# Performance work log

Hardware: AMD Instinct MI355X
Metric: run time of the kernel (lower is better)

## Reference

```python
import jax, jax.numpy as jnp
import numpy as np


def setup_inputs() -> dict:
    key = jax.random.key(0)
    ks = jax.random.split(key, 5)
    B, C, H, W = 4, 256, 48, 48
    x = jax.random.normal(ks[0], (B, C, H, W), dtype=jnp.float32)
    w_qkv = jax.random.normal(ks[1], (3 * C, C), dtype=jnp.float32) * (C ** -0.5)
    b_qkv = jax.random.normal(ks[2], (3 * C,), dtype=jnp.float32) * 0.02
    w_proj = jax.random.normal(ks[3], (C, C), dtype=jnp.float32) * (C ** -0.5)
    b_proj = jax.random.normal(ks[4], (C,), dtype=jnp.float32) * 0.02
    return {"x": x, "w_qkv": w_qkv, "b_qkv": b_qkv, "w_proj": w_proj, "b_proj": b_proj, "num_heads": 4}


def reference(x, w_qkv, b_qkv, w_proj, b_proj, num_heads):
    B, C, H, W = x.shape
    N = H * W
    hd = C // num_heads
    # NOTE: original uses full-dim scale, not head_dim
    scale = C ** -0.5
    # 1x1 conv == channel matmul
    qkv = jnp.einsum('bchw,oc->bohw', x, w_qkv) + b_qkv[None, :, None, None]
    qkv = qkv.reshape(B, 3, num_heads, hd, N)
    q = qkv[:, 0].transpose(0, 1, 3, 2)  # [B, h, N, d]
    k = qkv[:, 1]                         # [B, h, d, N]
    v = qkv[:, 2].transpose(0, 1, 3, 2)  # [B, h, N, d]
    attn = jax.nn.softmax((q @ k) * scale, axis=-1)  # [B, h, N, N]
    out = attn @ v                        # [B, h, N, d]
    out = out.transpose(0, 1, 3, 2).reshape(B, C, H, W)
    return jnp.einsum('bchw,oc->bohw', out, w_proj) + b_proj[None, :, None, None]
```

## Files before the change

### kernel.cpp

```cpp
#include <hip/hip_runtime.h>
#include <hip/hip_bf16.h>
#include <stdint.h>

typedef unsigned short u16;
typedef unsigned int u32;
typedef __attribute__((ext_vector_type(8))) short bf16x8;
typedef __attribute__((ext_vector_type(4))) float f32x4;
typedef __attribute__((ext_vector_type(4))) unsigned short u16x4;

#define MFMA16 __builtin_amdgcn_mfma_f32_16x16x32_bf16

static constexpr int Bb = 4;
static constexpr int Cc = 256;
static constexpr int NHh = 4;
static constexpr int HDd = 64;
static constexpr int Nn = 2304;

__device__ __forceinline__ u16 f2bf(float f) {
  u32 u = __builtin_bit_cast(u32, f);
  u32 r = u + 0x7fffu + ((u >> 16) & 1u);
  return (u16)(r >> 16);
}

__device__ __forceinline__ u32 cvtpk(float a, float b) {
  u32 r;
  asm("v_cvt_pk_bf16_f32 %0, %1, %2" : "=v"(r) : "v"(a), "v"(b));
  return r;
}

__device__ __forceinline__ float blo(u32 u) { return __builtin_bit_cast(float, u << 16); }
__device__ __forceinline__ float bhi(u32 u) { return __builtin_bit_cast(float, u & 0xffff0000u); }

__device__ __forceinline__ void async16(const void* g, void* l) {
  __builtin_amdgcn_global_load_lds(
      (const __attribute__((address_space(1))) u32*)g,
      (__attribute__((address_space(3))) u32*)l, 16, 0, 0);
}

__global__ __launch_bounds__(256) void k_prep(const float* __restrict__ wq,
                                              const float* __restrict__ wp,
                                              u16* __restrict__ wqb,
                                              u16* __restrict__ wpb) {
  int i = blockIdx.x * 256 + threadIdx.x;
  if (i < 3 * Cc * Cc) wqb[i] = f2bf(wq[i]);
  if (i < Cc * Cc)     wpb[i] = f2bf(wp[i]);
}

__global__ __launch_bounds__(256) void k_qkv(const u16* __restrict__ wqb,
                                             const float* __restrict__ x,
                                             const float* __restrict__ bqkv,
                                             u16* __restrict__ qT, u16* __restrict__ kT,
                                             u16* __restrict__ vT) {
  __shared__ float tile[64][65];
  __shared__ u16 Bs[64 * 256];
  int n0 = blockIdx.y * 64, b = blockIdx.z;
  int t = threadIdx.x, w = t >> 6, l = t & 63, g = l >> 4, li = l & 15;
  char* BsB = (char*)Bs;
#pragma unroll
  for (int cc = 0; cc < 4; ++cc) {
#pragma unroll
    for (int i = 0; i < 16; ++i) {
      int cl = i * 4 + w;
      tile[cl][l] = x[((size_t)(b * Cc + cc * 64 + cl)) * Nn + n0 + l];
    }
    __syncthreads();
#pragma unroll
    for (int i = 0; i < 16; ++i) {
      int nr = i * 4 + w;
      int byte = nr * 512 + ((2 * (cc * 64 + l)) ^ ((nr & 7) << 4));
      *(u16*)(BsB + byte) = f2bf(tile[l][nr]);
    }
    __syncthreads();
  }
  const float qs = 0.0625f * 1.44269504088896340736f;
#pragma unroll
  for (int p = 0; p < 2; ++p) {
    int o0 = blockIdx.x * 128 + p * 64;
    const u16* Arow = wqb + (size_t)(o0 + w * 16 + li) * Cc;
    f32x4 acc[4] = {};
#pragma unroll
    for (int s = 0; s < 8; ++s) {
      bf16x8 a = *(const bf16x8*)(Arow + s * 32 + g * 8);
#pragma unroll
      for (int nt = 0; nt < 4; ++nt) {
        int row = nt * 16 + li;
        const char* bp_ = (const char*)Bs + row * 512 + ((s * 64 + g * 16) ^ ((row & 7) << 4));
        bf16x8 bb = *(const bf16x8*)bp_;
        acc[nt] = MFMA16(a, bb, acc[nt], 0, 0, 0);
      }
    }
    int which = o0 >> 8;
    int hh = (o0 >> 6) & 3;
    int bh = b * NHh + hh;
    int dbase = w * 16 + g * 4;
#pragma unroll
    for (int nt = 0; nt < 4; ++nt) {
      int n = n0 + nt * 16 + li;
      float v0 = acc[nt][0] + bqkv[o0 + dbase + 0];
      float v1 = acc[nt][1] + bqkv[o0 + dbase + 1];
      float v2 = acc[nt][2] + bqkv[o0 + dbase + 2];
      float v3 = acc[nt][3] + bqkv[o0 + dbase + 3];
      if (which == 0) {
        u16x4 pq = {f2bf(v0 * qs), f2bf(v1 * qs), f2bf(v2 * qs), f2bf(v3 * qs)};
        *(u16x4*)(qT + ((size_t)bh * Nn + n) * HDd + dbase) = pq;
      } else if (which == 1) {
        u16x4 pk = {f2bf(v0), f2bf(v1), f2bf(v2), f2bf(v3)};
        *(u16x4*)(kT + ((size_t)bh * Nn + n) * HDd + dbase) = pk;
      } else {
        vT[((size_t)bh * HDd + dbase + 0) * Nn + n] = f2bf(v0);
        vT[((size_t)bh * HDd + dbase + 1) * Nn + n] = f2bf(v1);
        vT[((size_t)bh * HDd + dbase + 2) * Nn + n] = f2bf(v2);
        vT[((size_t)bh * HDd + dbase + 3) * Nn + n] = f2bf(v3);
      }
    }
  }
}

__global__ __launch_bounds__(192) void k_attn(const u16* __restrict__ qT,
                                              const u16* __restrict__ kT,
                                              const u16* __restrict__ vT,
                                              u16* __restrict__ attP,
                                              float* __restrict__ lsumP) {
  __shared__ u16 Ks[2][32 * 64];
  __shared__ u16 Vs[2][64 * 32];
  __shared__ u16 Ps[3][32 * 32];
  int L = blockIdx.x;
  int xcd = L & 7, r = L >> 3;
  int bh = 2 * xcd + (r >= 96 ? 1 : 0);
  int r2 = (r >= 96) ? r - 96 : r;
  int quarter = r2 / 24;
  int qb = r2 % 24;
  int t = threadIdx.x, w = t / 64, l = t & 63, g = l >> 4, li = l & 15;
  int q0 = qb * 96 + w * 32;
  const u16* qr0 = qT + ((size_t)bh * Nn + q0 + li) * HDd;
  const u16* qr1 = qT + ((size_t)bh * Nn + q0 + 16 + li) * HDd;
  bf16x8 bq[2][2];
  bq[0][0] = *(const bf16x8*)(qr0 + g * 8);
  bq[0][1] = *(const bf16x8*)(qr0 + 32 + g * 8);
  bq[1][0] = *(const bf16x8*)(qr1 + g * 8);
  bq[1][1] = *(const bf16x8*)(qr1 + 32 + g * 8);
  const short one = (short)0x3F80;
  bf16x8 ONES = {one, one, one, one, one, one, one, one};
  f32x4 acc[2][4] = {};
  f32x4 acc_l[2] = {};
  const char* kbh = (const char*)(kT + (size_t)bh * Nn * HDd);
  const char* vbh = (const char*)(vT + (size_t)bh * HDd * Nn);
  char* PsB = (char*)(&Ps[w][0]);
  int sw_li = (li & 7) << 4;
  int sw2   = ((li >> 1) & 3) << 4;

  const char* sp[3];
  int sd[3];
  ptrdiff_t sstr[3];
  bool son[3], svv[3];
#pragma unroll
  for (int it = 0; it < 3; ++it) {
    int gg = w * 3 + it;
    son[it] = (gg < 8);
    int c = gg * 64 + l;
    if (c < 256) {
      int key = c >> 3, c8 = c & 7;
      sp[it] = kbh + (size_t)(quarter * 576 + key) * 128 + ((c8 * 16) ^ ((key & 7) << 4));
      sd[it] = c * 16; sstr[it] = 32 * 128; svv[it] = false;
    } else {
      int cv = c - 256, d = cv >> 2, c4 = cv & 3;
      sp[it] = vbh + (size_t)d * (Nn * 2) + quarter * 1152 +
               ((c4 * 16) ^ (((d >> 1) & 3) << 4));
      sd[it] = cv * 16; sstr[it] = 32 * 2; svv[it] = true;
    }
  }

  auto STAGE = [&](int buf) {
    char* kdst = (char*)(&Ks[0][0]) + buf * 4096;
    char* vdst = (char*)(&Vs[0][0]) + buf * 4096;
#pragma unroll
    for (int it = 0; it < 3; ++it) {
      if (son[it]) {
        async16(sp[it], (svv[it] ? vdst : kdst) + sd[it]);
        sp[it] += sstr[it];
      }
    }
  };

  STAGE(0);
  int cur = 0;
  for (int kb = 0; kb < 18; ++kb) {
    __syncthreads();
    if (kb + 1 < 18) STAGE(cur ^ 1);

    const char* Kc = (const char*)(&Ks[0][0]) + cur * 4096;
    const char* Vc = (const char*)(&Vs[0][0]) + cur * 4096;

    f32x4 s[2][2];
    __builtin_amdgcn_s_setprio(1);
#pragma unroll
    for (int kt = 0; kt < 2; ++kt) {
      const char* kr = Kc + (kt * 16 + li) * 128;
      bf16x8 a0 = *(const bf16x8*)(kr + ((g * 16) ^ sw_li));
      bf16x8 a1 = *(const bf16x8*)(kr + ((64 + g * 16) ^ sw_li));
#pragma unroll
      for (int st = 0; st < 2; ++st) {
        f32x4 z = {};
        z = MFMA16(a0, bq[st][0], z, 0, 0, 0);
        z = MFMA16(a1, bq[st][1], z, 0, 0, 0);
        s[st][kt] = z;
      }
    }
    __builtin_amdgcn_s_setprio(0);

#pragma unroll
    for (int st = 0; st < 2; ++st) {
#pragma unroll
      for (int kt = 0; kt < 2; ++kt)
#pragma unroll
        for (int j = 0; j < 4; ++j) s[st][kt][j] = exp2f(s[st][kt][j]);
      int rq = st * 16 + li;
#pragma unroll
      for (int kt = 0; kt < 2; ++kt) {
        uint2 pk;
        pk.x = cvtpk(s[st][kt][0], s[st][kt][1]);
        pk.y = cvtpk(s[st][kt][2], s[st][kt][3]);
        *(uint2*)(PsB + rq * 64 + ((kt * 32 + g * 8) ^ sw2)) = pk;
      }
    }
    bf16x8 pa[2];
    pa[0] = *(const bf16x8*)(PsB + (0 * 16 + li) * 64 + ((g * 16) ^ sw2));
    pa[1] = *(const bf16x8*)(PsB + (1 * 16 + li) * 64 + ((g * 16) ^ sw2));
    __builtin_amdgcn_s_setprio(1);
    acc_l[0] = MFMA16(pa[0], ONES, acc_l[0], 0, 0, 0);
    acc_l[1] = MFMA16(pa[1], ONES, acc_l[1], 0, 0, 0);
#pragma unroll
    for (int dt = 0; dt < 4; ++dt) {
      const char* vr = Vc + (dt * 16 + li) * 64;
      bf16x8 v0 = *(const bf16x8*)(vr + ((g * 16) ^ sw2));
      acc[0][dt] = MFMA16(pa[0], v0, acc[0][dt], 0, 0, 0);
      acc[1][dt] = MFMA16(pa[1], v0, acc[1][dt], 0, 0, 0);
    }
    __builtin_amdgcn_s_setprio(0);
    cur ^= 1;
  }
  u16* ap = attP + (size_t)quarter * (Bb * Nn * Cc);
  float* lp = lsumP + quarter * (Bb * NHh * Nn);
  if (li == 0) {
#pragma unroll
    for (int st = 0; st < 2; ++st)
#pragma unroll
      for (int j = 0; j < 4; ++j)
        lp[bh * Nn + q0 + st * 16 + g * 4 + j] = acc_l[st][j];
  }
  int b = bh >> 2, hh = bh & 3;
#pragma unroll
  for (int st = 0; st < 2; ++st)
#pragma unroll
    for (int dt = 0; dt < 4; ++dt) {
      int cidx = hh * 64 + dt * 16 + li;
#pragma unroll
      for (int j = 0; j < 4; ++j) {
        ap[((size_t)(b * Nn + q0 + st * 16 + g * 4 + j)) * Cc + cidx] = f2bf(acc[st][dt][j]);
      }
    }
}

__global__ __launch_bounds__(256) void k_merge(const u16* __restrict__ attP,
                                               const float* __restrict__ lsumP,
                                               u16* __restrict__ attT) {
  int gid = blockIdx.x * 256 + threadIdx.x;
  int base = gid * 8;
  int bidx = base / (Nn * Cc);
  int rem = base - bidx * (Nn * Cc);
  int n = rem >> 8, c = rem & 255;
  int hh = c >> 6;
  int lidx = (bidx * NHh + hh) * Nn + n;
  const int LQ = Bb * NHh * Nn;
  float inv = 1.0f / (lsumP[lidx] + lsumP[LQ + lidx] +
                      lsumP[2 * LQ + lidx] + lsumP[3 * LQ + lidx]);
  const size_t QSZ = (size_t)Bb * Nn * Cc;
  uint4 p0 = *(const uint4*)(attP + base);
  uint4 p1 = *(const uint4*)(attP + QSZ + base);
  uint4 p2 = *(const uint4*)(attP + 2 * QSZ + base);
  uint4 p3 = *(const uint4*)(attP + 3 * QSZ + base);
  uint4 o;
  o.x = cvtpk((blo(p0.x) + blo(p1.x) + blo(p2.x) + blo(p3.x)) * inv,
              (bhi(p0.x) + bhi(p1.x) + bhi(p2.x) + bhi(p3.x)) * inv);
  o.y = cvtpk((blo(p0.y) + blo(p1.y) + blo(p2.y) + blo(p3.y)) * inv,
              (bhi(p0.y) + bhi(p1.y) + bhi(p2.y) + bhi(p3.y)) * inv);
  o.z = cvtpk((blo(p0.z) + blo(p1.z) + blo(p2.z) + blo(p3.z)) * inv,
              (bhi(p0.z) + bhi(p1.z) + bhi(p2.z) + bhi(p3.z)) * inv);
  o.w = cvtpk((blo(p0.w) + blo(p1.w) + blo(p2.w) + blo(p3.w)) * inv,
              (bhi(p0.w) + bhi(p1.w) + bhi(p2.w) + bhi(p3.w)) * inv);
  *(uint4*)(attT + base) = o;
}

__global__ __launch_bounds__(256) void k_proj(const u16* __restrict__ wpb,
                                              const u16* __restrict__ attT,
                                              const float* __restrict__ bp,
                                              float* __restrict__ out) {
  __shared__ u16 Bs[32 * 256];
  int bx = blockIdx.x, n0 = blockIdx.y * 32, b = blockIdx.z;
  int t = threadIdx.x, w = t >> 6, l = t & 63, g = l >> 4, li = l & 15;
#pragma unroll
  for (int it = 0; it < 4; ++it) {
    int ch = it * 256 + t;
    int row = ch >> 5, c16 = ch & 31;
    const char* src = (const char*)attT + ((size_t)(b * Nn + n0 + row)) * 512 +
                      ((c16 * 16) ^ ((row & 7) << 4));
    async16(src, (char*)Bs + (it * 256 + (t & ~63)) * 16);
  }
  const u16* Arow0 = wpb + (size_t)(bx * 128 + w * 16 + li) * Cc;
  const u16* Arow1 = Arow0 + (size_t)64 * Cc;
  __syncthreads();
  f32x4 acc[2][2] = {};
#pragma unroll
  for (int s = 0; s < 8; ++s) {
    bf16x8 a0 = *(const bf16x8*)(Arow0 + s * 32 + g * 8);
    bf16x8 a1 = *(const bf16x8*)(Arow1 + s * 32 + g * 8);
#pragma unroll
    for (int nt = 0; nt < 2; ++nt) {
      int row = nt * 16 + li;
      const char* bp_ = (const char*)Bs + row * 512 + ((s * 64 + g * 16) ^ ((row & 7) << 4));
      bf16x8 bb = *(const bf16x8*)bp_;
      acc[0][nt] = MFMA16(a0, bb, acc[0][nt], 0, 0, 0);
      acc[1][nt] = MFMA16(a1, bb, acc[1][nt], 0, 0, 0);
    }
  }
#pragma unroll
  for (int nt = 0; nt < 2; ++nt) {
    int n = n0 + nt * 16 + li;
#pragma unroll
    for (int p = 0; p < 2; ++p) {
      int obase = bx * 128 + p * 64 + w * 16 + g * 4;
#pragma unroll
      for (int j = 0; j < 4; ++j) {
        out[((size_t)(b * Cc + obase + j)) * Nn + n] = acc[p][nt][j] + bp[obase + j];
      }
    }
  }
}

extern "C" void kernel_launch(void* const* d_in, const int* in_sizes, int n_in,
                              void* d_out, int out_size, void* d_ws, size_t ws_size,
                              hipStream_t stream) {
  const float* x     = (const float*)d_in[0];
  const float* wqkv  = (const float*)d_in[1];
  const float* bqkv  = (const float*)d_in[2];
  const float* wproj = (const float*)d_in[3];
  const float* bproj = (const float*)d_in[4];
  float* out = (float*)d_out;

  u16* ws    = (u16*)d_ws;
  u16* wq_bf = ws;
  u16* wp_bf = wq_bf + 196608;
  u16* qT    = wp_bf + 65536;
  u16* kT    = qT + 2359296;
  u16* vT    = kT + 2359296;
  u16* attP  = vT + 2359296;
  float* lsumP = (float*)(attP + 4 * 2359296);
  u16* attT  = qT;

  k_prep<<<dim3(768), dim3(256), 0, stream>>>(wqkv, wproj, wq_bf, wp_bf);
  k_qkv<<<dim3(6, 36, 4), dim3(256), 0, stream>>>(wq_bf, x, bqkv, qT, kT, vT);
  k_attn<<<dim3(1536), dim3(192), 0, stream>>>(qT, kT, vT, attP, lsumP);
  k_merge<<<dim3(1152), dim3(256), 0, stream>>>(attP, lsumP, attT);
  k_proj<<<dim3(2, 72, 4), dim3(256), 0, stream>>>(wp_bf, attT, bproj, out);
}
```

Baseline: 86.82 us.

## Split keys six ways and feed P to MFMA from registers, dropping LDS roundtrip

Raises the key-split count from four to six, so the attention grid grows to 2304 blocks, each handling 12 key tiles instead of 18. The merge kernel now sums six partial outputs and row sums. The P matrix no longer goes through shared memory. The S accumulator layout is reused directly as the B operand of 16x16x16 bf16 MFMAs, with V as the A operand. The output becomes transposed, so it is stored with vectorized 4-wide writes. This trades an extra workspace partial, more merge traffic and twice as many smaller MFMAs for removing the LDS round trip and gaining parallelism.

```diff
diff --git a/kernel.cpp b/kernel.cpp
--- a/kernel.cpp
+++ b/kernel.cpp
@@ -5,16 +5,39 @@
 typedef unsigned short u16;
 typedef unsigned int u32;
 typedef __attribute__((ext_vector_type(8))) short bf16x8;
+typedef __attribute__((ext_vector_type(4))) short bf16x4;
 typedef __attribute__((ext_vector_type(4))) float f32x4;
+typedef __attribute__((ext_vector_type(2))) unsigned int u32x2;
 typedef __attribute__((ext_vector_type(4))) unsigned short u16x4;
 
 #define MFMA16 __builtin_amdgcn_mfma_f32_16x16x32_bf16
+
+#if __has_builtin(__builtin_amdgcn_mfma_f32_16x16x16bf16_1k)
+__device__ __forceinline__ f32x4 MFMAK16(u32x2 a, u32x2 b, f32x4 c) {
+  return __builtin_amdgcn_mfma_f32_16x16x16bf16_1k(
+      __builtin_bit_cast(bf16x4, a), __builtin_bit_cast(bf16x4, b), c, 0, 0, 0);
+}
+#elif __has_builtin(__builtin_amdgcn_mfma_f32_16x16x16_bf16)
+typedef __attribute__((ext_vector_type(4))) __bf16 bf16v4;
+__device__ __forceinline__ f32x4 MFMAK16(u32x2 a, u32x2 b, f32x4 c) {
+  return __builtin_amdgcn_mfma_f32_16x16x16_bf16(
+      __builtin_bit_cast(bf16v4, a), __builtin_bit_cast(bf16v4, b), c, 0, 0, 0);
+}
+#else
+__device__ __forceinline__ f32x4 MFMAK16(u32x2 a, u32x2 b, f32x4 c) {
+  f32x4 d;
+  asm("s_nop 1\n\tv_mfma_f32_16x16x16_bf16 %0, %1, %2, %3"
+      : "=v"(d) : "v"(a), "v"(b), "v"(c));
+  return d;
+}
+#endif
 
 static constexpr int Bb = 4;
 static constexpr int Cc = 256;
 static constexpr int NHh = 4;
 static constexpr int HDd = 64;
 static constexpr int Nn = 2304;
+static constexpr int NSPLIT = 6;
 
 __device__ __forceinline__ u16 f2bf(float f) {
   u32 u = __builtin_bit_cast(u32, f);
@@ -116,20 +139,19 @@
   }
 }
 
-__global__ __launch_bounds__(192) void k_attn(const u16* __restrict__ qT,
-                                              const u16* __restrict__ kT,
-                                              const u16* __restrict__ vT,
-                                              u16* __restrict__ attP,
-                                              float* __restrict__ lsumP) {
+__global__ __launch_bounds__(192, 7) void k_attn(const u16* __restrict__ qT,
+                                                 const u16* __restrict__ kT,
+                                                 const u16* __restrict__ vT,
+                                                 u16* __restrict__ attP,
+                                                 float* __restrict__ lsumP) {
   __shared__ u16 Ks[2][32 * 64];
   __shared__ u16 Vs[2][64 * 32];
-  __shared__ u16 Ps[3][32 * 32];
   int L = blockIdx.x;
-  int xcd = L & 7, r = L >> 3;
-  int bh = 2 * xcd + (r >= 96 ? 1 : 0);
-  int r2 = (r >= 96) ? r - 96 : r;
-  int quarter = r2 / 24;
-  int qb = r2 % 24;
+  int xcd = L & 7, r2 = L >> 3;
+  int bh = 2 * xcd + (r2 >= 144 ? 1 : 0);
+  int rr = (r2 >= 144) ? r2 - 144 : r2;
+  int sext = rr / 24;
+  int qb = rr % 24;
   int t = threadIdx.x, w = t / 64, l = t & 63, g = l >> 4, li = l & 15;
   int q0 = qb * 96 + w * 32;
   const u16* qr0 = qT + ((size_t)bh * Nn + q0 + li) * HDd;
@@ -139,13 +161,12 @@
   bq[0][1] = *(const bf16x8*)(qr0 + 32 + g * 8);
   bq[1][0] = *(const bf16x8*)(qr1 + g * 8);
   bq[1][1] = *(const bf16x8*)(qr1 + 32 + g * 8);
-  const short one = (short)0x3F80;
-  bf16x8 ONES = {one, one, one, one, one, one, one, one};
+  const u32 one2 = 0x3F803F80u;
+  u32x2 ONESK = {one2, one2};
   f32x4 acc[2][4] = {};
   f32x4 acc_l[2] = {};
   const char* kbh = (const char*)(kT + (size_t)bh * Nn * HDd);
   const char* vbh = (const char*)(vT + (size_t)bh * HDd * Nn);
-  char* PsB = (char*)(&Ps[w][0]);
   int sw_li = (li & 7) << 4;
   int sw2   = ((li >> 1) & 3) << 4;
 
@@ -160,11 +181,11 @@
     int c = gg * 64 + l;
     if (c < 256) {
       int key = c >> 3, c8 = c & 7;
-      sp[it] = kbh + (size_t)(quarter * 576 + key) * 128 + ((c8 * 16) ^ ((key & 7) << 4));
+      sp[it] = kbh + (size_t)(sext * 384 + key) * 128 + ((c8 * 16) ^ ((key & 7) << 4));
       sd[it] = c * 16; sstr[it] = 32 * 128; svv[it] = false;
     } else {
       int cv = c - 256, d = cv >> 2, c4 = cv & 3;
-      sp[it] = vbh + (size_t)d * (Nn * 2) + quarter * 1152 +
+      sp[it] = vbh + (size_t)d * (Nn * 2) + sext * 768 +
                ((c4 * 16) ^ (((d >> 1) & 3) << 4));
       sd[it] = cv * 16; sstr[it] = 32 * 2; svv[it] = true;
     }
@@ -184,9 +205,9 @@
 
   STAGE(0);
   int cur = 0;
-  for (int kb = 0; kb < 18; ++kb) {
+  for (int kb = 0; kb < 12; ++kb) {
     __syncthreads();
-    if (kb + 1 < 18) STAGE(cur ^ 1);
+    if (kb + 1 < 12) STAGE(cur ^ 1);
 
     const char* Kc = (const char*)(&Ks[0][0]) + cur * 4096;
     const char* Vc = (const char*)(&Vs[0][0]) + cur * 4096;
@@ -208,57 +229,53 @@
     }
     __builtin_amdgcn_s_setprio(0);
 
-#pragma unroll
-    for (int st = 0; st < 2; ++st) {
-#pragma unroll
-      for (int kt = 0; kt < 2; ++kt)
+    u32x2 pb[2][2];
+#pragma unroll
+    for (int st = 0; st < 2; ++st)
+#pragma unroll
+      for (int kt = 0; kt < 2; ++kt) {
 #pragma unroll
         for (int j = 0; j < 4; ++j) s[st][kt][j] = exp2f(s[st][kt][j]);
-      int rq = st * 16 + li;
-#pragma unroll
-      for (int kt = 0; kt < 2; ++kt) {
-        uint2 pk;
-        pk.x = cvtpk(s[st][kt][0], s[st][kt][1]);
-        pk.y = cvtpk(s[st][kt][2], s[st][kt][3]);
-        *(uint2*)(PsB + rq * 64 + ((kt * 32 + g * 8) ^ sw2)) = pk;
-      }
-    }
-    bf16x8 pa[2];
-    pa[0] = *(const bf16x8*)(PsB + (0 * 16 + li) * 64 + ((g * 16) ^ sw2));
-    pa[1] = *(const bf16x8*)(PsB + (1 * 16 + li) * 64 + ((g * 16) ^ sw2));
+        pb[st][kt][0] = cvtpk(s[st][kt][0], s[st][kt][1]);
+        pb[st][kt][1] = cvtpk(s[st][kt][2], s[st][kt][3]);
+      }
+
     __builtin_amdgcn_s_setprio(1);
-    acc_l[0] = MFMA16(pa[0], ONES, acc_l[0], 0, 0, 0);
-    acc_l[1] = MFMA16(pa[1], ONES, acc_l[1], 0, 0, 0);
+    acc_l[0] = MFMAK16(ONESK, pb[0][0], acc_l[0]);
+    acc_l[0] = MFMAK16(ONESK, pb[0][1], acc_l[0]);
+    acc_l[1] = MFMAK16(ONESK, pb[1][0], acc_l[1]);
+    acc_l[1] = MFMAK16(ONESK, pb[1][1], acc_l[1]);
 #pragma unroll
     for (int dt = 0; dt < 4; ++dt) {
       const char* vr = Vc + (dt * 16 + li) * 64;
-      bf16x8 v0 = *(const bf16x8*)(vr + ((g * 16) ^ sw2));
-      acc[0][dt] = MFMA16(pa[0], v0, acc[0][dt], 0, 0, 0);
-      acc[1][dt] = MFMA16(pa[1], v0, acc[1][dt], 0, 0, 0);
+#pragma unroll
+      for (int kt = 0; kt < 2; ++kt) {
+        u32x2 vf = *(const u32x2*)(vr + ((kt * 32 + g * 8) ^ sw2));
+        acc[0][dt] = MFMAK16(vf, pb[0][kt], acc[0][dt]);
+        acc[1][dt] = MFMAK16(vf, pb[1][kt], acc[1][dt]);
+      }
     }
     __builtin_amdgcn_s_setprio(0);
     cur ^= 1;
   }
-  u16* ap = attP + (size_t)quarter * (Bb * Nn * Cc);
-  float* lp = lsumP + quarter * (Bb * NHh * Nn);
-  if (li == 0) {
-#pragma unroll
-    for (int st = 0; st < 2; ++st)
-#pragma unroll
-      for (int j = 0; j < 4; ++j)
-        lp[bh * Nn + q0 + st * 16 + g * 4 + j] = acc_l[st][j];
+  asm volatile("s_nop 7\n\ts_nop 7");
+  u16* ap = attP + (size_t)sext * (Bb * Nn * Cc);
+  float* lp = lsumP + sext * (Bb * NHh * Nn);
+  if (l < 16) {
+    lp[bh * Nn + q0 + li] = acc_l[0][0];
+    lp[bh * Nn + q0 + 16 + li] = acc_l[1][0];
   }
   int b = bh >> 2, hh = bh & 3;
 #pragma unroll
-  for (int st = 0; st < 2; ++st)
+  for (int st = 0; st < 2; ++st) {
+    int q = q0 + st * 16 + li;
 #pragma unroll
     for (int dt = 0; dt < 4; ++dt) {
-      int cidx = hh * 64 + dt * 16 + li;
-#pragma unroll
-      for (int j = 0; j < 4; ++j) {
-        ap[((size_t)(b * Nn + q0 + st * 16 + g * 4 + j)) * Cc + cidx] = f2bf(acc[st][dt][j]);
-      }
-    }
+      u16x4 pk = {f2bf(acc[st][dt][0]), f2bf(acc[st][dt][1]),
+                  f2bf(acc[st][dt][2]), f2bf(acc[st][dt][3])};
+      *(u16x4*)(ap + ((size_t)(b * Nn + q)) * Cc + hh * 64 + dt * 16 + g * 4) = pk;
+    }
+  }
 }
 
 __global__ __launch_bounds__(256) void k_merge(const u16* __restrict__ attP,
@@ -272,22 +289,25 @@
   int hh = c >> 6;
   int lidx = (bidx * NHh + hh) * Nn + n;
   const int LQ = Bb * NHh * Nn;
-  float inv = 1.0f / (lsumP[lidx] + lsumP[LQ + lidx] +
-                      lsumP[2 * LQ + lidx] + lsumP[3 * LQ + lidx]);
+  float lsum = 0.f;
+#pragma unroll
+  for (int q = 0; q < NSPLIT; ++q) lsum += lsumP[q * LQ + lidx];
+  float inv = 1.0f / lsum;
   const size_t QSZ = (size_t)Bb * Nn * Cc;
-  uint4 p0 = *(const uint4*)(attP + base);
-  uint4 p1 = *(const uint4*)(attP + QSZ + base);
-  uint4 p2 = *(const uint4*)(attP + 2 * QSZ + base);
-  uint4 p3 = *(const uint4*)(attP + 3 * QSZ + base);
+  float s0 = 0, s1 = 0, s2 = 0, s3 = 0, s4 = 0, s5 = 0, s6 = 0, s7 = 0;
+#pragma unroll
+  for (int q = 0; q < NSPLIT; ++q) {
+    uint4 p = *(const uint4*)(attP + q * QSZ + base);
+    s0 += blo(p.x); s1 += bhi(p.x);
+    s2 += blo(p.y); s3 += bhi(p.y);
+    s4 += blo(p.z); s5 += bhi(p.z);
+    s6 += blo(p.w); s7 += bhi(p.w);
+  }
   uint4 o;
-  o.x = cvtpk((blo(p0.x) + blo(p1.x) + blo(p2.x) + blo(p3.x)) * inv,
-              (bhi(p0.x) + bhi(p1.x) + bhi(p2.x) + bhi(p3.x)) * inv);
-  o.y = cvtpk((blo(p0.y) + blo(p1.y) + blo(p2.y) + blo(p3.y)) * inv,
-              (bhi(p0.y) + bhi(p1.y) + bhi(p2.y) + bhi(p3.y)) * inv);
-  o.z = cvtpk((blo(p0.z) + blo(p1.z) + blo(p2.z) + blo(p3.z)) * inv,
-              (bhi(p0.z) + bhi(p1.z) + bhi(p2.z) + bhi(p3.z)) * inv);
-  o.w = cvtpk((blo(p0.w) + blo(p1.w) + blo(p2.w) + blo(p3.w)) * inv,
-              (bhi(p0.w) + bhi(p1.w) + bhi(p2.w) + bhi(p3.w)) * inv);
+  o.x = cvtpk(s0 * inv, s1 * inv);
+  o.y = cvtpk(s2 * inv, s3 * inv);
+  o.z = cvtpk(s4 * inv, s5 * inv);
+  o.w = cvtpk(s6 * inv, s7 * inv);
   *(uint4*)(attT + base) = o;
 }
 
@@ -354,12 +374,12 @@
   u16* kT    = qT + 2359296;
   u16* vT    = kT + 2359296;
   u16* attP  = vT + 2359296;
-  float* lsumP = (float*)(attP + 4 * 2359296);
+  float* lsumP = (float*)(attP + NSPLIT * 2359296);
   u16* attT  = qT;
 
   k_prep<<<dim3(768), dim3(256), 0, stream>>>(wqkv, wproj, wq_bf, wp_bf);
   k_qkv<<<dim3(6, 36, 4), dim3(256), 0, stream>>>(wq_bf, x, bqkv, qT, kT, vT);
-  k_attn<<<dim3(1536), dim3(192), 0, stream>>>(qT, kT, vT, attP, lsumP);
+  k_attn<<<dim3(2304), dim3(192), 0, stream>>>(qT, kT, vT, attP, lsumP);
   k_merge<<<dim3(1152), dim3(256), 0, stream>>>(attP, lsumP, attT);
   k_proj<<<dim3(2, 72, 4), dim3(256), 0, stream>>>(wp_bf, attT, bproj, out);
 }
```

New measurement: 270.8 us. +211.9%, slower.
